# Performance work log

Hardware: AMD Instinct MI355X
Metric: run time of the kernel (lower is better)

Reference implementation:

```python
import jax, jax.numpy as jnp
import numpy as np

EPS = 1e-8      # laplace_transform epsilon
RC = 0.5        # residual_coff
L = 2           # num_layers
NU, NB, NI, D = 100000, 30000, 50000, 128
E_UB, E_UI, E_BI = 300000, 500000, 500000


def _l2norm(x):
    # F.normalize(x, p=2, dim=1)
    n = jnp.linalg.norm(x, axis=1, keepdims=True)
    return x / jnp.maximum(n, 1e-12)


def _spmm(rows, cols, vals, feats, n):
    # sparse (COO) matmul: out[r] += vals[e] * feats[cols[e]]
    return jax.ops.segment_sum(vals[:, None] * feats[cols], rows, num_segments=n)


def _sym_norm_graph(u, v, na, nb):
    # bipartite block matrix [[0, B],[B^T, 0]] with D^-1/2 A D^-1/2 normalization
    rows = jnp.concatenate([u, v + na])
    cols = jnp.concatenate([v + na, u])
    deg = jax.ops.segment_sum(jnp.ones(rows.shape[0], jnp.float32), rows,
                              num_segments=na + nb)
    dinv = 1.0 / (jnp.sqrt(deg) + EPS)
    vals = dinv[rows] * dinv[cols]
    return rows, cols, vals


def _one_propagate(rows, cols, vals, afeat, bfeat):
    n = afeat.shape[0] + bfeat.shape[0]
    feats = jnp.concatenate([afeat, bfeat], axis=0)
    ini = _l2norm(feats)
    acc = feats  # all_feats starts with raw feats, summed at the end
    for i in range(L):
        feats = _spmm(rows, cols, vals, feats, n)
        feats = (feats + RC * ini) / (i + 2)
        feats = _l2norm(feats)
        acc = acc + feats
    return acc[:afeat.shape[0]], acc[afeat.shape[0]:]


def setup_inputs() -> dict:
    key = jax.random.key(0)
    ks = jax.random.split(key, 10)
    return {
        "users_feat": jax.random.normal(ks[0], (NU, D), jnp.float32) * 0.1,
        "bundles_feat": jax.random.normal(ks[1], (NB, D), jnp.float32) * 0.1,
        "items_feat": jax.random.normal(ks[2], (NI, D), jnp.float32) * 0.1,
        "bi_vals": jax.random.uniform(ks[3], (E_BI,), jnp.float32),
        "ub_u": jax.random.randint(ks[4], (E_UB,), 0, NU),
        "ub_b": jax.random.randint(ks[5], (E_UB,), 0, NB),
        "ui_u": jax.random.randint(ks[6], (E_UI,), 0, NU),
        "ui_i": jax.random.randint(ks[7], (E_UI,), 0, NI),
        "bi_b": jax.random.randint(ks[8], (E_BI,), 0, NB),
        "bi_i": jax.random.randint(ks[9], (E_BI,), 0, NI),
    }


def reference(users_feat, bundles_feat, items_feat, bi_vals,
              ub_u, ub_b, ui_u, ui_i, bi_b, bi_i):
    nu, nb, ni = users_feat.shape[0], bundles_feat.shape[0], items_feat.shape[0]
    # UB (history) propagation
    r, c, v = _sym_norm_graph(ub_u, ub_b, nu, nb)
    hist_users, hist_bundles = _one_propagate(r, c, v, users_feat, bundles_feat)
    # UI (affinity) propagation
    r, c, v = _sym_norm_graph(ui_u, ui_i, nu, ni)
    aff_users, ui_items = _one_propagate(r, c, v, users_feat, items_feat)
    # BI aggregation: bundles x items sparse graph @ item features
    aff_bundles = _spmm(bi_b, bi_i, bi_vals, ui_items, nb)
    # concat [aff_users, hist_users, aff_bundles, hist_bundles] along rows
    return jnp.concatenate([aff_users, hist_users, aff_bundles, hist_bundles], axis=0)
```

## Files before the change

kernel.cpp:

```cpp
#include <hip/hip_runtime.h>

#define FD   128
#define FDH  64
#define EPSN 1e-8f
#define RCC  0.5f
#define SCAN_TPB 256
#define SCAN_ELEMS 1024

typedef unsigned int uint;
typedef unsigned short u16;
typedef unsigned char u8;
typedef float fx2 __attribute__((ext_vector_type(2)));

__device__ __forceinline__ float wave_sum(float x) {
#pragma unroll
    for (int off = 32; off > 0; off >>= 1) x += __shfl_xor(x, off);
    return x;
}

__device__ __forceinline__ uint packbf2(float a, float b) {
    uint ua = __float_as_uint(a); ua += 0x7fffu + ((ua >> 16) & 1u);
    uint ub = __float_as_uint(b); ub += 0x7fffu + ((ub >> 16) & 1u);
    return (ua >> 16) | (ub & 0xffff0000u);
}
__device__ __forceinline__ float2 unpackbf2(uint v) {
    return make_float2(__uint_as_float(v << 16), __uint_as_float(v & 0xffff0000u));
}
__device__ __forceinline__ u16 packfp8(float a, float b) {
    return (u16)__builtin_amdgcn_cvt_pk_fp8_f32(a, b, 0, false);
}

__global__ void passA(const int* __restrict__ ub_u, const int* __restrict__ ub_b,
                      const int* __restrict__ ui_u, const int* __restrict__ ui_i,
                      const int* __restrict__ bi_b, const int* __restrict__ bi_i,
                      const float* __restrict__ uf, const float* __restrict__ bf,
                      const float* __restrict__ itf,
                      int E_UB, int E_UI, int E_BI, int NU, int NB, int n1, int n2, int NT,
                      int nblk_edges,
                      int* __restrict__ head, int2* __restrict__ pairLL,
                      uint* __restrict__ fini16, float* __restrict__ normf) {
    if ((int)blockIdx.x < nblk_edges) {
        int e = blockIdx.x * blockDim.x + threadIdx.x;
        if (e < E_UB) {
            int a = ub_u[e], b = ub_b[e] + NU;
            int s0 = 2 * e;
            int p0 = atomicExch(&head[a], s0);
            int p1 = atomicExch(&head[b], s0 + 1);
            ((int4*)pairLL)[e] = make_int4(p0, b, p1, a);
        } else if (e < E_UB + E_UI) {
            int f = e - E_UB;
            int a = ui_u[f], bl = ui_i[f] + NU;
            int s0 = 2 * E_UB + 2 * f;
            int p0 = atomicExch(&head[n1 + a], s0);
            int p1 = atomicExch(&head[n1 + bl], s0 + 1);
            ((int4*)pairLL)[E_UB + f] = make_int4(p0, bl, p1, a);
        } else if (e < E_UB + E_UI + E_BI) {
            int g = e - E_UB - E_UI;
            int s = 2 * E_UB + 2 * E_UI + g;
            int p = atomicExch(&head[n1 + n2 + bi_b[g]], s);
            pairLL[s] = make_int2(p, bi_i[g]);
        }
    } else {
        int w = (((int)blockIdx.x - nblk_edges) * blockDim.x + threadIdx.x) >> 6;
        int lane = threadIdx.x & 63;
        if (w >= NT) return;
        const float* src = (w < NU) ? uf + (size_t)w * FD
                         : (w < NU + NB) ? bf + (size_t)(w - NU) * FD
                         : itf + (size_t)(w - NU - NB) * FD;
        float2 x = ((const float2*)src)[lane];
        float ss = wave_sum(x.x * x.x + x.y * x.y);
        float nrm = sqrtf(ss);
        float inv = 1.0f / fmaxf(nrm, 1e-12f);
        fini16[(size_t)w * FDH + lane] = packbf2(x.x * inv, x.y * inv);
        if (lane == 0) normf[w] = nrm;
    }
}

__global__ void passB(const int* __restrict__ head, const int2* __restrict__ pairLL,
                      int NN, int n12, int* __restrict__ deg, float* __restrict__ dinv) {
    int r = blockIdx.x * blockDim.x + threadIdx.x;
    if (r > NN) return;
    if (r == NN) { deg[NN] = 0; return; }
    int c = 0;
    int s = head[r];
    while (s >= 0) { c++; s = pairLL[s].x; }
    deg[r] = c;
    if (r < n12) dinv[r] = 1.0f / (sqrtf((float)c) + EPSN);
}

__global__ void conv_g8(const uint* __restrict__ fini16, const float* __restrict__ normf,
                        const float* __restrict__ dinv,
                        int n1, int NU, int NB, int n12, u16* __restrict__ g8) {
    int w = (blockIdx.x * blockDim.x + threadIdx.x) >> 6;
    int lane = threadIdx.x & 63;
    if (w >= n12) return;
    int node = (w < n1) ? w : ((w - n1 < NU) ? (w - n1) : (w - n1 + NB));
    float sc = dinv[w] * normf[node];
    float2 f = unpackbf2(fini16[(size_t)node * FDH + lane]);
    g8[(size_t)w * FDH + lane] = packfp8(f.x * sc, f.y * sc);
}

__global__ void scan_a(const int* __restrict__ in, int* __restrict__ out,
                       int* __restrict__ bsum, int nelem) {
    __shared__ int tsum[SCAN_TPB];
    int tid = threadIdx.x;
    int base = blockIdx.x * SCAN_ELEMS + tid * 4;
    int v0 = (base + 0 < nelem) ? in[base + 0] : 0;
    int v1 = (base + 1 < nelem) ? in[base + 1] : 0;
    int v2 = (base + 2 < nelem) ? in[base + 2] : 0;
    int v3 = (base + 3 < nelem) ? in[base + 3] : 0;
    int s = v0 + v1 + v2 + v3;
    tsum[tid] = s;
    __syncthreads();
    for (int off = 1; off < SCAN_TPB; off <<= 1) {
        int y = (tid >= off) ? tsum[tid - off] : 0;
        __syncthreads();
        tsum[tid] += y;
        __syncthreads();
    }
    int excl = tsum[tid] - s;
    if (tid == SCAN_TPB - 1) bsum[blockIdx.x] = tsum[SCAN_TPB - 1];
    if (base + 0 < nelem) out[base + 0] = excl;
    excl += v0;
    if (base + 1 < nelem) out[base + 1] = excl;
    excl += v1;
    if (base + 2 < nelem) out[base + 2] = excl;
    excl += v2;
    if (base + 3 < nelem) out[base + 3] = excl;
}

__global__ void scan_b(int* __restrict__ bsum, int nb) {
    __shared__ int sm[512];
    int tid = threadIdx.x;
    int v = (tid < nb) ? bsum[tid] : 0;
    sm[tid] = v;
    __syncthreads();
    for (int off = 1; off < 512; off <<= 1) {
        int y = (tid >= off) ? sm[tid - off] : 0;
        __syncthreads();
        sm[tid] += y;
        __syncthreads();
    }
    if (tid < nb) bsum[tid] = sm[tid] - v;
}

__global__ void scan_c(int* __restrict__ out, const int* __restrict__ bsum, int nelem) {
    int base = blockIdx.x * SCAN_ELEMS + threadIdx.x * 4;
    int add = bsum[blockIdx.x];
#pragma unroll
    for (int k = 0; k < 4; ++k)
        if (base + k < nelem) out[base + k] += add;
}

__global__ void passC(const int* __restrict__ head, const int2* __restrict__ pairLL,
                      const int* __restrict__ rowptr, const float* __restrict__ bi_vals,
                      int NN, int n12, int S1,
                      int* __restrict__ cols, float* __restrict__ wts) {
    int r = blockIdx.x * blockDim.x + threadIdx.x;
    if (r >= NN) return;
    int pos = rowptr[r];
    int s = head[r];
    if (r < n12) {
        while (s >= 0) { int2 p = pairLL[s]; cols[pos++] = p.y << 7; s = p.x; }
    } else {
        while (s >= 0) {
            int2 p = pairLL[s];
            cols[pos] = p.y << 8;
            wts[pos - S1] = bi_vals[s - S1];
            pos++; s = p.x;
        }
    }
}

#define GATHER_FP8(TAB)                                                          \
    float a0 = 0.f, a1 = 0.f, a2 = 0.f, a3 = 0.f;                                \
    for (int cs = s; cs < e; cs += 64) {                                         \
        int cnt = e - cs; if (cnt > 64) cnt = 64;                                \
        int colv = (lane < cnt) ? cols[cs + lane] : 0;                           \
        int p = 0;                                                               \
        for (; 2 * p + 8 <= cnt; p += 4) {                                       \
            int o0 = __shfl(colv, 2 * p + h);                                    \
            int o1 = __shfl(colv, 2 * p + 2 + h);                                \
            int o2 = __shfl(colv, 2 * p + 4 + h);                                \
            int o3 = __shfl(colv, 2 * p + 6 + h);                                \
            uint x0 = *(const uint*)(TAB + o0);                                  \
            uint x1 = *(const uint*)(TAB + o1);                                  \
            uint x2 = *(const uint*)(TAB + o2);                                  \
            uint x3 = *(const uint*)(TAB + o3);                                  \
            fx2 p0 = __builtin_amdgcn_cvt_pk_f32_fp8((int)x0, false);            \
            fx2 r0 = __builtin_amdgcn_cvt_pk_f32_fp8((int)x0, true);             \
            fx2 p1 = __builtin_amdgcn_cvt_pk_f32_fp8((int)x1, false);            \
            fx2 r1 = __builtin_amdgcn_cvt_pk_f32_fp8((int)x1, true);             \
            fx2 p2 = __builtin_amdgcn_cvt_pk_f32_fp8((int)x2, false);            \
            fx2 r2 = __builtin_amdgcn_cvt_pk_f32_fp8((int)x2, true);             \
            fx2 p3 = __builtin_amdgcn_cvt_pk_f32_fp8((int)x3, false);            \
            fx2 r3 = __builtin_amdgcn_cvt_pk_f32_fp8((int)x3, true);             \
            a0 += p0.x + p1.x + p2.x + p3.x;                                     \
            a1 += p0.y + p1.y + p2.y + p3.y;                                     \
            a2 += r0.x + r1.x + r2.x + r3.x;                                     \
            a3 += r0.y + r1.y + r2.y + r3.y;                                     \
        }                                                                        \
        for (; 2 * p + 2 <= cnt; ++p) {                                          \
            int o = __shfl(colv, 2 * p + h);                                     \
            uint x = *(const uint*)(TAB + o);                                    \
            fx2 pp = __builtin_amdgcn_cvt_pk_f32_fp8((int)x, false);             \
            fx2 rr = __builtin_amdgcn_cvt_pk_f32_fp8((int)x, true);              \
            a0 += pp.x; a1 += pp.y; a2 += rr.x; a3 += rr.y;                      \
        }                                                                        \
        if (2 * p < cnt) {                                                       \
            int o = __shfl(colv, 2 * p);                                         \
            if (h == 0) {                                                        \
                uint x = *(const uint*)(TAB + o);                                \
                fx2 pp = __builtin_amdgcn_cvt_pk_f32_fp8((int)x, false);         \
                fx2 rr = __builtin_amdgcn_cvt_pk_f32_fp8((int)x, true);          \
                a0 += pp.x; a1 += pp.y; a2 += rr.x; a3 += rr.y;                  \
            }                                                                    \
        }                                                                        \
    }                                                                            \
    a0 += __shfl_xor(a0, 32); a1 += __shfl_xor(a1, 32);                          \
    a2 += __shfl_xor(a2, 32); a3 += __shfl_xor(a3, 32);

__global__ void spmm_L1(const int* __restrict__ rowptr, const int* __restrict__ cols,
                        const float* __restrict__ dinv, const float* __restrict__ normf,
                        const uint* __restrict__ fini16, const u16* __restrict__ g8,
                        uint* __restrict__ facc16, uint* __restrict__ fX8,
                        int n1, int NU, int NB, int n12) {
    int w = (blockIdx.x * blockDim.x + threadIdx.x) >> 6;
    int lane = threadIdx.x & 63;
    if (w >= n12) return;
    int h = lane >> 5, q = lane & 31;
    int s = rowptr[w], e = rowptr[w + 1];
    bool ui = (w >= n1);
    int node = ui ? ((w - n1 < NU) ? (w - n1) : (w - n1 + NB)) : w;
    float dr = dinv[w];
    uint2 iu = ((const uint2*)(fini16 + (size_t)node * FDH))[q];
    float nr = normf[node];
    const u8* tab = (const u8*)g8 + ((size_t)(ui ? n1 : 0) << 7) + (q << 2);
    GATHER_FP8(tab)
    float2 i01 = unpackbf2(iu.x), i23 = unpackbf2(iu.y);
    float v0 = (dr * a0 + RCC * i01.x) * 0.5f;
    float v1 = (dr * a1 + RCC * i01.y) * 0.5f;
    float v2 = (dr * a2 + RCC * i23.x) * 0.5f;
    float v3 = (dr * a3 + RCC * i23.y) * 0.5f;
    float sq = v0 * v0 + v1 * v1 + v2 * v2 + v3 * v3;
#pragma unroll
    for (int off = 16; off > 0; off >>= 1) sq += __shfl_xor(sq, off);
    float inv = 1.0f / fmaxf(sqrtf(sq), 1e-12f);
    v0 *= inv; v1 *= inv; v2 *= inv; v3 *= inv;
    if (h == 0) {
        uint2 fa;
        fa.x = packbf2(fmaf(i01.x, nr, v0), fmaf(i01.y, nr, v1));
        fa.y = packbf2(fmaf(i23.x, nr, v2), fmaf(i23.y, nr, v3));
        ((uint2*)(facc16 + (size_t)w * FDH))[q] = fa;
        int xu = __builtin_amdgcn_cvt_pk_fp8_f32(v0 * dr, v1 * dr, 0, false);
        xu = __builtin_amdgcn_cvt_pk_fp8_f32(v2 * dr, v3 * dr, xu, true);
        fX8[(size_t)w * 32 + q] = (uint)xu;
    }
}

__global__ void spmm_L2(const int* __restrict__ rowptr, const int* __restrict__ cols,
                        const float* __restrict__ dinv, const uint* __restrict__ fini16,
                        const uint* __restrict__ facc16, const uint* __restrict__ fX8,
                        uint* __restrict__ items16, float* __restrict__ outp,
                        int n1, int NU, int NB, int n12) {
    int w = (blockIdx.x * blockDim.x + threadIdx.x) >> 6;
    int lane = threadIdx.x & 63;
    if (w >= n12) return;
    int h = lane >> 5, q = lane & 31;
    int s = rowptr[w], e = rowptr[w + 1];
    bool ui = (w >= n1);
    int node = ui ? ((w - n1 < NU) ? (w - n1) : (w - n1 + NB)) : w;
    float dr = dinv[w];
    uint2 iu = ((const uint2*)(fini16 + (size_t)node * FDH))[q];
    uint2 au = ((const uint2*)(facc16 + (size_t)w * FDH))[q];
    const u8* tab = (const u8*)fX8 + ((size_t)(ui ? n1 : 0) << 7) + (q << 2);
    GATHER_FP8(tab)
    float2 i01 = unpackbf2(iu.x), i23 = unpackbf2(iu.y);
    float v0 = (dr * a0 + RCC * i01.x) * (1.0f / 3.0f);
    float v1 = (dr * a1 + RCC * i01.y) * (1.0f / 3.0f);
    float v2 = (dr * a2 + RCC * i23.x) * (1.0f / 3.0f);
    float v3 = (dr * a3 + RCC * i23.y) * (1.0f / 3.0f);
    float sq = v0 * v0 + v1 * v1 + v2 * v2 + v3 * v3;
#pragma unroll
    for (int off = 16; off > 0; off >>= 1) sq += __shfl_xor(sq, off);
    float inv = 1.0f / fmaxf(sqrtf(sq), 1e-12f);
    v0 *= inv; v1 *= inv; v2 *= inv; v3 *= inv;
    float2 a01 = unpackbf2(au.x), a23 = unpackbf2(au.y);
    float n0 = a01.x + v0, o1v = a01.y + v1, n2v = a23.x + v2, n3 = a23.y + v3;
    if (h == 0) {
        if (!ui) {
            size_t dst = (w < NU) ? (size_t)(NU + w) : (size_t)(2 * NU + NB + (w - NU));
            ((float4*)(outp + dst * FD))[q] = make_float4(n0, o1v, n2v, n3);
        } else {
            int l = w - n1;
            if (l < NU) {
                ((float4*)(outp + (size_t)l * FD))[q] = make_float4(n0, o1v, n2v, n3);
            } else {
                uint2 it;
                it.x = packbf2(n0, o1v);
                it.y = packbf2(n2v, n3);
                ((uint2*)(items16 + (size_t)(l - NU) * FDH))[q] = it;
            }
        }
    }
}

__global__ void bi_gather(const int* __restrict__ rowptr, const int* __restrict__ cols,
                          const float* __restrict__ wts, int S1,
                          const uint* __restrict__ items16,
                          float* __restrict__ outb, int nb) {
    int w = (blockIdx.x * blockDim.x + threadIdx.x) >> 6;
    int lane = threadIdx.x & 63;
    if (w >= nb) return;
    int h = lane >> 5, q = lane & 31;
    int s = rowptr[w], e = rowptr[w + 1];
    const u8* tab = (const u8*)items16 + (q << 3);
    float a0 = 0.f, a1 = 0.f, a2 = 0.f, a3 = 0.f;
    for (int cs = s; cs < e; cs += 64) {
        int cnt = e - cs; if (cnt > 64) cnt = 64;
        int colv = (lane < cnt) ? cols[cs + lane] : 0;
        float wtv = (lane < cnt) ? wts[cs + lane - S1] : 0.0f;
        int p = 0;
        for (; 2 * p + 8 <= cnt; p += 4) {
            int o0 = __shfl(colv, 2 * p + h);
            int o1 = __shfl(colv, 2 * p + 2 + h);
            int o2 = __shfl(colv, 2 * p + 4 + h);
            int o3 = __shfl(colv, 2 * p + 6 + h);
            float w0 = __shfl(wtv, 2 * p + h);
            float w1 = __shfl(wtv, 2 * p + 2 + h);
            float w2 = __shfl(wtv, 2 * p + 4 + h);
            float w3 = __shfl(wtv, 2 * p + 6 + h);
            uint2 x0 = *(const uint2*)(tab + o0);
            uint2 x1 = *(const uint2*)(tab + o1);
            uint2 x2 = *(const uint2*)(tab + o2);
            uint2 x3 = *(const uint2*)(tab + o3);
            float2 f;
            f = unpackbf2(x0.x); a0 = fmaf(w0, f.x, a0); a1 = fmaf(w0, f.y, a1);
            f = unpackbf2(x0.y); a2 = fmaf(w0, f.x, a2); a3 = fmaf(w0, f.y, a3);
            f = unpackbf2(x1.x); a0 = fmaf(w1, f.x, a0); a1 = fmaf(w1, f.y, a1);
            f = unpackbf2(x1.y); a2 = fmaf(w1, f.x, a2); a3 = fmaf(w1, f.y, a3);
            f = unpackbf2(x2.x); a0 = fmaf(w2, f.x, a0); a1 = fmaf(w2, f.y, a1);
            f = unpackbf2(x2.y); a2 = fmaf(w2, f.x, a2); a3 = fmaf(w2, f.y, a3);
            f = unpackbf2(x3.x); a0 = fmaf(w3, f.x, a0); a1 = fmaf(w3, f.y, a1);
            f = unpackbf2(x3.y); a2 = fmaf(w3, f.x, a2); a3 = fmaf(w3, f.y, a3);
        }
        for (; 2 * p + 2 <= cnt; ++p) {
            int o = __shfl(colv, 2 * p + h);
            float wt = __shfl(wtv, 2 * p + h);
            uint2 x = *(const uint2*)(tab + o);
            float2 f;
            f = unpackbf2(x.x); a0 = fmaf(wt, f.x, a0); a1 = fmaf(wt, f.y, a1);
            f = unpackbf2(x.y); a2 = fmaf(wt, f.x, a2); a3 = fmaf(wt, f.y, a3);
        }
        if (2 * p < cnt) {
            int o = __shfl(colv, 2 * p);
            float wt = __shfl(wtv, 2 * p);
            if (h == 0) {
                uint2 x = *(const uint2*)(tab + o);
                float2 f;
                f = unpackbf2(x.x); a0 = fmaf(wt, f.x, a0); a1 = fmaf(wt, f.y, a1);
                f = unpackbf2(x.y); a2 = fmaf(wt, f.x, a2); a3 = fmaf(wt, f.y, a3);
            }
        }
    }
    a0 += __shfl_xor(a0, 32); a1 += __shfl_xor(a1, 32);
    a2 += __shfl_xor(a2, 32); a3 += __shfl_xor(a3, 32);
    if (h == 0)
        ((float4*)(outb + (size_t)w * FD))[q] = make_float4(a0, a1, a2, a3);
}

extern "C" void kernel_launch(void* const* d_in, const int* in_sizes, int n_in,
                              void* d_out, int out_size, void* d_ws, size_t ws_size,
                              hipStream_t stream) {
    const float* users   = (const float*)d_in[0];
    const float* bundles = (const float*)d_in[1];
    const float* items   = (const float*)d_in[2];
    const float* bi_vals = (const float*)d_in[3];
    const int* ub_u = (const int*)d_in[4];
    const int* ub_b = (const int*)d_in[5];
    const int* ui_u = (const int*)d_in[6];
    const int* ui_i = (const int*)d_in[7];
    const int* bi_b = (const int*)d_in[8];
    const int* bi_i = (const int*)d_in[9];

    const int NU = in_sizes[0] / FD;
    const int NB = in_sizes[1] / FD;
    const int NI = in_sizes[2] / FD;
    const int E_BI = in_sizes[3];
    const int E_UB = in_sizes[4];
    const int E_UI = in_sizes[6];
    float* out = (float*)d_out;

    const int n1 = NU + NB, n2 = NU + NI;
    const int n12 = n1 + n2;
    const int NT = NU + NB + NI;
    const int NN = n12 + NB;
    const int S1 = 2 * E_UB + 2 * E_UI;
    const int TOT = S1 + E_BI;
    const int ETOT = E_UB + E_UI + E_BI;

    uint* fini16   = (uint*)d_ws;
    uint* facc16   = fini16 + (size_t)NT * FDH;
    uint* items16  = facc16 + (size_t)n12 * FDH;
    u16* g8        = (u16*)(items16 + (size_t)NI * FDH);
    uint* fX8      = (uint*)(g8 + (size_t)n12 * FDH);
    float* normf   = (float*)(fX8 + (size_t)n12 * 32);
    float* dinv    = normf + NT;
    float* wts     = dinv + n12;
    int* deg       = (int*)(wts + E_BI);
    int* rowptr    = deg + (NN + 1);
    int* head      = rowptr + (NN + 1);
    int* bsum      = head + NN;
    int* cols      = bsum + 512;
    int2* pairLL   = (int2*)((((size_t)(cols + TOT)) + 15) & ~(size_t)15);

    dim3 blk(256);
    auto rows_grid = [](int n) { return dim3((unsigned)((n + 3) / 4)); };
    auto thr_grid  = [](int n) { return dim3((unsigned)((n + 255) / 256)); };

    hipMemsetAsync(head, 0xFF, (size_t)NN * 4, stream);
    int nblk_edges = (ETOT + 255) / 256;
    int nblk_prep  = (NT + 3) / 4;
    passA<<<dim3((unsigned)(nblk_edges + nblk_prep)), blk, 0, stream>>>(
        ub_u, ub_b, ui_u, ui_i, bi_b, bi_i, users, bundles, items,
        E_UB, E_UI, E_BI, NU, NB, n1, n2, NT, nblk_edges,
        head, pairLL, fini16, normf);
    passB<<<thr_grid(NN + 1), blk, 0, stream>>>(head, pairLL, NN, n12, deg, dinv);
    conv_g8<<<rows_grid(n12), blk, 0, stream>>>(fini16, normf, dinv, n1, NU, NB, n12, g8);
    {
        int nelem = NN + 1;
        int nblk = (nelem + SCAN_ELEMS - 1) / SCAN_ELEMS;
        scan_a<<<dim3((unsigned)nblk), dim3(SCAN_TPB), 0, stream>>>(deg, rowptr, bsum, nelem);
        scan_b<<<dim3(1), dim3(512), 0, stream>>>(bsum, nblk);
        scan_c<<<dim3((unsigned)nblk), dim3(SCAN_TPB), 0, stream>>>(rowptr, bsum, nelem);
    }
    passC<<<thr_grid(NN), blk, 0, stream>>>(head, pairLL, rowptr, bi_vals,
                                            NN, n12, S1, cols, wts);

    spmm_L1<<<rows_grid(n12), blk, 0, stream>>>(rowptr, cols, dinv, normf,
                                                fini16, g8, facc16, fX8, n1, NU, NB, n12);
    spmm_L2<<<rows_grid(n12), blk, 0, stream>>>(rowptr, cols, dinv, fini16,
                                                facc16, fX8, items16, out, n1, NU, NB, n12);
    bi_gather<<<rows_grid(NB), blk, 0, stream>>>(rowptr + n12, cols, wts, S1, items16,
        out + (size_t)2 * NU * FD, NB);
}
```

Before: 675.9 us.

## Process two rows per wavefront, fuse conv_g8 into passC, pack BI cols+weights

```diff
diff --git a/kernel.cpp b/kernel.cpp
--- a/kernel.cpp
+++ b/kernel.cpp
@@ -88,18 +88,6 @@
     if (r < n12) dinv[r] = 1.0f / (sqrtf((float)c) + EPSN);
 }
 
-__global__ void conv_g8(const uint* __restrict__ fini16, const float* __restrict__ normf,
-                        const float* __restrict__ dinv,
-                        int n1, int NU, int NB, int n12, u16* __restrict__ g8) {
-    int w = (blockIdx.x * blockDim.x + threadIdx.x) >> 6;
-    int lane = threadIdx.x & 63;
-    if (w >= n12) return;
-    int node = (w < n1) ? w : ((w - n1 < NU) ? (w - n1) : (w - n1 + NB));
-    float sc = dinv[w] * normf[node];
-    float2 f = unpackbf2(fini16[(size_t)node * FDH + lane]);
-    g8[(size_t)w * FDH + lane] = packfp8(f.x * sc, f.y * sc);
-}
-
 __global__ void scan_a(const int* __restrict__ in, int* __restrict__ out,
                        int* __restrict__ bsum, int nelem) {
     __shared__ int tsum[SCAN_TPB];
@@ -152,109 +140,127 @@
         if (base + k < nelem) out[base + k] += add;
 }
 
-__global__ void passC(const int* __restrict__ head, const int2* __restrict__ pairLL,
-                      const int* __restrict__ rowptr, const float* __restrict__ bi_vals,
-                      int NN, int n12, int S1,
-                      int* __restrict__ cols, float* __restrict__ wts) {
-    int r = blockIdx.x * blockDim.x + threadIdx.x;
-    if (r >= NN) return;
-    int pos = rowptr[r];
-    int s = head[r];
-    if (r < n12) {
-        while (s >= 0) { int2 p = pairLL[s]; cols[pos++] = p.y << 7; s = p.x; }
+__global__ void passC_conv(const int* __restrict__ head, const int2* __restrict__ pairLL,
+                           const int* __restrict__ rowptr, const float* __restrict__ bi_vals,
+                           int NN, int n12, int S1,
+                           int* __restrict__ cols, int2* __restrict__ bi2,
+                           const uint* __restrict__ fini16, const float* __restrict__ normf,
+                           const float* __restrict__ dinv,
+                           int n1, int NU, int NB, u16* __restrict__ g8, int nblkC) {
+    if ((int)blockIdx.x < nblkC) {
+        int r = blockIdx.x * blockDim.x + threadIdx.x;
+        if (r >= NN) return;
+        int pos = rowptr[r];
+        int s = head[r];
+        if (r < n12) {
+            while (s >= 0) { int2 p = pairLL[s]; cols[pos++] = p.y << 7; s = p.x; }
+        } else {
+            while (s >= 0) {
+                int2 p = pairLL[s];
+                bi2[pos - S1] = make_int2(p.y << 8, __float_as_int(bi_vals[s - S1]));
+                pos++; s = p.x;
+            }
+        }
     } else {
-        while (s >= 0) {
-            int2 p = pairLL[s];
-            cols[pos] = p.y << 8;
-            wts[pos - S1] = bi_vals[s - S1];
-            pos++; s = p.x;
-        }
-    }
-}
-
-#define GATHER_FP8(TAB)                                                          \
-    float a0 = 0.f, a1 = 0.f, a2 = 0.f, a3 = 0.f;                                \
-    for (int cs = s; cs < e; cs += 64) {                                         \
-        int cnt = e - cs; if (cnt > 64) cnt = 64;                                \
-        int colv = (lane < cnt) ? cols[cs + lane] : 0;                           \
+        int w = (((int)blockIdx.x - nblkC) * blockDim.x + threadIdx.x) >> 6;
+        int lane = threadIdx.x & 63;
+        if (w >= n12) return;
+        int node = (w < n1) ? w : ((w - n1 < NU) ? (w - n1) : (w - n1 + NB));
+        float sc = dinv[w] * normf[node];
+        float2 f = unpackbf2(fini16[(size_t)node * FDH + lane]);
+        g8[(size_t)w * FDH + lane] = packfp8(f.x * sc, f.y * sc);
+    }
+}
+
+#define ACC8(XU)  {                                                              \
+    fx2 _pa = __builtin_amdgcn_cvt_pk_f32_fp8((int)(XU).x, false);               \
+    fx2 _pb = __builtin_amdgcn_cvt_pk_f32_fp8((int)(XU).x, true);                \
+    fx2 _pc = __builtin_amdgcn_cvt_pk_f32_fp8((int)(XU).y, false);               \
+    fx2 _pd = __builtin_amdgcn_cvt_pk_f32_fp8((int)(XU).y, true);                \
+    a0 += _pa.x; a1 += _pa.y; a2 += _pb.x; a3 += _pb.y;                          \
+    a4 += _pc.x; a5 += _pc.y; a6 += _pd.x; a7 += _pd.y; }
+
+#define GATHER8(TAB)                                                             \
+    float a0=0.f,a1=0.f,a2=0.f,a3=0.f,a4=0.f,a5=0.f,a6=0.f,a7=0.f;               \
+    {                                                                            \
+      int base = lane & 32;                                                      \
+      for (int cs = s; cs < e; cs += 32) {                                       \
+        int cnt = e - cs; if (cnt > 32) cnt = 32;                                \
+        int colv = (l31 < cnt) ? cols[cs + l31] : 0;                             \
         int p = 0;                                                               \
         for (; 2 * p + 8 <= cnt; p += 4) {                                       \
-            int o0 = __shfl(colv, 2 * p + h);                                    \
-            int o1 = __shfl(colv, 2 * p + 2 + h);                                \
-            int o2 = __shfl(colv, 2 * p + 4 + h);                                \
-            int o3 = __shfl(colv, 2 * p + 6 + h);                                \
-            uint x0 = *(const uint*)(TAB + o0);                                  \
-            uint x1 = *(const uint*)(TAB + o1);                                  \
-            uint x2 = *(const uint*)(TAB + o2);                                  \
-            uint x3 = *(const uint*)(TAB + o3);                                  \
-            fx2 p0 = __builtin_amdgcn_cvt_pk_f32_fp8((int)x0, false);            \
-            fx2 r0 = __builtin_amdgcn_cvt_pk_f32_fp8((int)x0, true);             \
-            fx2 p1 = __builtin_amdgcn_cvt_pk_f32_fp8((int)x1, false);            \
-            fx2 r1 = __builtin_amdgcn_cvt_pk_f32_fp8((int)x1, true);             \
-            fx2 p2 = __builtin_amdgcn_cvt_pk_f32_fp8((int)x2, false);            \
-            fx2 r2 = __builtin_amdgcn_cvt_pk_f32_fp8((int)x2, true);             \
-            fx2 p3 = __builtin_amdgcn_cvt_pk_f32_fp8((int)x3, false);            \
-            fx2 r3 = __builtin_amdgcn_cvt_pk_f32_fp8((int)x3, true);             \
-            a0 += p0.x + p1.x + p2.x + p3.x;                                     \
-            a1 += p0.y + p1.y + p2.y + p3.y;                                     \
-            a2 += r0.x + r1.x + r2.x + r3.x;                                     \
-            a3 += r0.y + r1.y + r2.y + r3.y;                                     \
+            int o0 = __shfl(colv, base + 2 * p + sub);                           \
+            int o1 = __shfl(colv, base + 2 * p + 2 + sub);                       \
+            int o2 = __shfl(colv, base + 2 * p + 4 + sub);                       \
+            int o3 = __shfl(colv, base + 2 * p + 6 + sub);                       \
+            uint2 x0 = *(const uint2*)(TAB + o0);                                \
+            uint2 x1 = *(const uint2*)(TAB + o1);                                \
+            uint2 x2 = *(const uint2*)(TAB + o2);                                \
+            uint2 x3 = *(const uint2*)(TAB + o3);                                \
+            ACC8(x0) ACC8(x1) ACC8(x2) ACC8(x3)                                  \
         }                                                                        \
         for (; 2 * p + 2 <= cnt; ++p) {                                          \
-            int o = __shfl(colv, 2 * p + h);                                     \
-            uint x = *(const uint*)(TAB + o);                                    \
-            fx2 pp = __builtin_amdgcn_cvt_pk_f32_fp8((int)x, false);             \
-            fx2 rr = __builtin_amdgcn_cvt_pk_f32_fp8((int)x, true);              \
-            a0 += pp.x; a1 += pp.y; a2 += rr.x; a3 += rr.y;                      \
+            int o = __shfl(colv, base + 2 * p + sub);                            \
+            uint2 x = *(const uint2*)(TAB + o);                                  \
+            ACC8(x)                                                              \
         }                                                                        \
         if (2 * p < cnt) {                                                       \
-            int o = __shfl(colv, 2 * p);                                         \
-            if (h == 0) {                                                        \
-                uint x = *(const uint*)(TAB + o);                                \
-                fx2 pp = __builtin_amdgcn_cvt_pk_f32_fp8((int)x, false);         \
-                fx2 rr = __builtin_amdgcn_cvt_pk_f32_fp8((int)x, true);          \
-                a0 += pp.x; a1 += pp.y; a2 += rr.x; a3 += rr.y;                  \
-            }                                                                    \
+            int o = __shfl(colv, base + 2 * p);                                  \
+            if (sub == 0) { uint2 x = *(const uint2*)(TAB + o); ACC8(x) }        \
         }                                                                        \
+      }                                                                          \
     }                                                                            \
-    a0 += __shfl_xor(a0, 32); a1 += __shfl_xor(a1, 32);                          \
-    a2 += __shfl_xor(a2, 32); a3 += __shfl_xor(a3, 32);
+    a0 += __shfl_xor(a0, 16); a1 += __shfl_xor(a1, 16);                          \
+    a2 += __shfl_xor(a2, 16); a3 += __shfl_xor(a3, 16);                          \
+    a4 += __shfl_xor(a4, 16); a5 += __shfl_xor(a5, 16);                          \
+    a6 += __shfl_xor(a6, 16); a7 += __shfl_xor(a7, 16);
 
 __global__ void spmm_L1(const int* __restrict__ rowptr, const int* __restrict__ cols,
                         const float* __restrict__ dinv, const float* __restrict__ normf,
                         const uint* __restrict__ fini16, const u16* __restrict__ g8,
                         uint* __restrict__ facc16, uint* __restrict__ fX8,
                         int n1, int NU, int NB, int n12) {
-    int w = (blockIdx.x * blockDim.x + threadIdx.x) >> 6;
+    int wv = (blockIdx.x * blockDim.x + threadIdx.x) >> 6;
     int lane = threadIdx.x & 63;
-    if (w >= n12) return;
-    int h = lane >> 5, q = lane & 31;
-    int s = rowptr[w], e = rowptr[w + 1];
-    bool ui = (w >= n1);
-    int node = ui ? ((w - n1 < NU) ? (w - n1) : (w - n1 + NB)) : w;
-    float dr = dinv[w];
-    uint2 iu = ((const uint2*)(fini16 + (size_t)node * FDH))[q];
+    int hw = lane >> 5, l31 = lane & 31, sub = (lane >> 4) & 1, t = lane & 15;
+    int r = 2 * wv + hw;
+    if (r >= n12) return;
+    int s = rowptr[r], e = rowptr[r + 1];
+    bool ui = (r >= n1);
+    int node = ui ? ((r - n1 < NU) ? (r - n1) : (r - n1 + NB)) : r;
+    float dr = dinv[r];
+    uint4 iu = ((const uint4*)(fini16 + (size_t)node * FDH))[t];
     float nr = normf[node];
-    const u8* tab = (const u8*)g8 + ((size_t)(ui ? n1 : 0) << 7) + (q << 2);
-    GATHER_FP8(tab)
+    const u8* tab = (const u8*)g8 + ((size_t)(ui ? n1 : 0) << 7) + (t << 3);
+    GATHER8(tab)
     float2 i01 = unpackbf2(iu.x), i23 = unpackbf2(iu.y);
+    float2 i45 = unpackbf2(iu.z), i67 = unpackbf2(iu.w);
     float v0 = (dr * a0 + RCC * i01.x) * 0.5f;
     float v1 = (dr * a1 + RCC * i01.y) * 0.5f;
     float v2 = (dr * a2 + RCC * i23.x) * 0.5f;
     float v3 = (dr * a3 + RCC * i23.y) * 0.5f;
-    float sq = v0 * v0 + v1 * v1 + v2 * v2 + v3 * v3;
+    float v4 = (dr * a4 + RCC * i45.x) * 0.5f;
+    float v5 = (dr * a5 + RCC * i45.y) * 0.5f;
+    float v6 = (dr * a6 + RCC * i67.x) * 0.5f;
+    float v7 = (dr * a7 + RCC * i67.y) * 0.5f;
+    float sq = v0*v0 + v1*v1 + v2*v2 + v3*v3 + v4*v4 + v5*v5 + v6*v6 + v7*v7;
 #pragma unroll
-    for (int off = 16; off > 0; off >>= 1) sq += __shfl_xor(sq, off);
+    for (int off = 8; off > 0; off >>= 1) sq += __shfl_xor(sq, off);
     float inv = 1.0f / fmaxf(sqrtf(sq), 1e-12f);
     v0 *= inv; v1 *= inv; v2 *= inv; v3 *= inv;
-    if (h == 0) {
-        uint2 fa;
+    v4 *= inv; v5 *= inv; v6 *= inv; v7 *= inv;
+    if (sub == 0) {
+        uint4 fa;
         fa.x = packbf2(fmaf(i01.x, nr, v0), fmaf(i01.y, nr, v1));
         fa.y = packbf2(fmaf(i23.x, nr, v2), fmaf(i23.y, nr, v3));
-        ((uint2*)(facc16 + (size_t)w * FDH))[q] = fa;
-        int xu = __builtin_amdgcn_cvt_pk_fp8_f32(v0 * dr, v1 * dr, 0, false);
-        xu = __builtin_amdgcn_cvt_pk_fp8_f32(v2 * dr, v3 * dr, xu, true);
-        fX8[(size_t)w * 32 + q] = (uint)xu;
+        fa.z = packbf2(fmaf(i45.x, nr, v4), fmaf(i45.y, nr, v5));
+        fa.w = packbf2(fmaf(i67.x, nr, v6), fmaf(i67.y, nr, v7));
+        ((uint4*)(facc16 + (size_t)r * FDH))[t] = fa;
+        int xa = __builtin_amdgcn_cvt_pk_fp8_f32(v0 * dr, v1 * dr, 0, false);
+        xa = __builtin_amdgcn_cvt_pk_fp8_f32(v2 * dr, v3 * dr, xa, true);
+        int xb = __builtin_amdgcn_cvt_pk_fp8_f32(v4 * dr, v5 * dr, 0, false);
+        xb = __builtin_amdgcn_cvt_pk_fp8_f32(v6 * dr, v7 * dr, xb, true);
+        ((uint2*)(fX8 + (size_t)r * 32))[t] = make_uint2((uint)xa, (uint)xb);
     }
 }
 
@@ -263,110 +269,121 @@
                         const uint* __restrict__ facc16, const uint* __restrict__ fX8,
                         uint* __restrict__ items16, float* __restrict__ outp,
                         int n1, int NU, int NB, int n12) {
-    int w = (blockIdx.x * blockDim.x + threadIdx.x) >> 6;
+    int wv = (blockIdx.x * blockDim.x + threadIdx.x) >> 6;
     int lane = threadIdx.x & 63;
-    if (w >= n12) return;
-    int h = lane >> 5, q = lane & 31;
-    int s = rowptr[w], e = rowptr[w + 1];
-    bool ui = (w >= n1);
-    int node = ui ? ((w - n1 < NU) ? (w - n1) : (w - n1 + NB)) : w;
-    float dr = dinv[w];
-    uint2 iu = ((const uint2*)(fini16 + (size_t)node * FDH))[q];
-    uint2 au = ((const uint2*)(facc16 + (size_t)w * FDH))[q];
-    const u8* tab = (const u8*)fX8 + ((size_t)(ui ? n1 : 0) << 7) + (q << 2);
-    GATHER_FP8(tab)
+    int hw = lane >> 5, l31 = lane & 31, sub = (lane >> 4) & 1, t = lane & 15;
+    int r = 2 * wv + hw;
+    if (r >= n12) return;
+    int s = rowptr[r], e = rowptr[r + 1];
+    bool ui = (r >= n1);
+    int node = ui ? ((r - n1 < NU) ? (r - n1) : (r - n1 + NB)) : r;
+    float dr = dinv[r];
+    uint4 iu = ((const uint4*)(fini16 + (size_t)node * FDH))[t];
+    uint4 au = ((const uint4*)(facc16 + (size_t)r * FDH))[t];
+    const u8* tab = (const u8*)fX8 + ((size_t)(ui ? n1 : 0) << 7) + (t << 3);
+    GATHER8(tab)
     float2 i01 = unpackbf2(iu.x), i23 = unpackbf2(iu.y);
+    float2 i45 = unpackbf2(iu.z), i67 = unpackbf2(iu.w);
     float v0 = (dr * a0 + RCC * i01.x) * (1.0f / 3.0f);
     float v1 = (dr * a1 + RCC * i01.y) * (1.0f / 3.0f);
     float v2 = (dr * a2 + RCC * i23.x) * (1.0f / 3.0f);
     float v3 = (dr * a3 + RCC * i23.y) * (1.0f / 3.0f);
-    float sq = v0 * v0 + v1 * v1 + v2 * v2 + v3 * v3;
+    float v4 = (dr * a4 + RCC * i45.x) * (1.0f / 3.0f);
+    float v5 = (dr * a5 + RCC * i45.y) * (1.0f / 3.0f);
+    float v6 = (dr * a6 + RCC * i67.x) * (1.0f / 3.0f);
+    float v7 = (dr * a7 + RCC * i67.y) * (1.0f / 3.0f);
+    float sq = v0*v0 + v1*v1 + v2*v2 + v3*v3 + v4*v4 + v5*v5 + v6*v6 + v7*v7;
 #pragma unroll
-    for (int off = 16; off > 0; off >>= 1) sq += __shfl_xor(sq, off);
+    for (int off = 8; off > 0; off >>= 1) sq += __shfl_xor(sq, off);
     float inv = 1.0f / fmaxf(sqrtf(sq), 1e-12f);
     v0 *= inv; v1 *= inv; v2 *= inv; v3 *= inv;
+    v4 *= inv; v5 *= inv; v6 *= inv; v7 *= inv;
     float2 a01 = unpackbf2(au.x), a23 = unpackbf2(au.y);
-    float n0 = a01.x + v0, o1v = a01.y + v1, n2v = a23.x + v2, n3 = a23.y + v3;
-    if (h == 0) {
+    float2 a45 = unpackbf2(au.z), a67 = unpackbf2(au.w);
+    float n0 = a01.x + v0, n1v = a01.y + v1, n2v = a23.x + v2, n3 = a23.y + v3;
+    float n4 = a45.x + v4, n5 = a45.y + v5, n6 = a67.x + v6, n7 = a67.y + v7;
+    if (sub == 0) {
         if (!ui) {
-            size_t dst = (w < NU) ? (size_t)(NU + w) : (size_t)(2 * NU + NB + (w - NU));
-            ((float4*)(outp + dst * FD))[q] = make_float4(n0, o1v, n2v, n3);
+            size_t dst = (r < NU) ? (size_t)(NU + r) : (size_t)(2 * NU + NB + (r - NU));
+            float* orow = outp + dst * FD;
+            ((float4*)orow)[2 * t]     = make_float4(n0, n1v, n2v, n3);
+            ((float4*)orow)[2 * t + 1] = make_float4(n4, n5, n6, n7);
         } else {
-            int l = w - n1;
+            int l = r - n1;
             if (l < NU) {
-                ((float4*)(outp + (size_t)l * FD))[q] = make_float4(n0, o1v, n2v, n3);
+                float* orow = outp + (size_t)l * FD;
+                ((float4*)orow)[2 * t]     = make_float4(n0, n1v, n2v, n3);
+                ((float4*)orow)[2 * t + 1] = make_float4(n4, n5, n6, n7);
             } else {
-                uint2 it;
-                it.x = packbf2(n0, o1v);
+                uint4 it;
+                it.x = packbf2(n0, n1v);
                 it.y = packbf2(n2v, n3);
-                ((uint2*)(items16 + (size_t)(l - NU) * FDH))[q] = it;
+                it.z = packbf2(n4, n5);
+                it.w = packbf2(n6, n7);
+                ((uint4*)(items16 + (size_t)(l - NU) * FDH))[t] = it;
             }
         }
     }
 }
 
-__global__ void bi_gather(const int* __restrict__ rowptr, const int* __restrict__ cols,
-                          const float* __restrict__ wts, int S1,
-                          const uint* __restrict__ items16,
+#define FMA8(XU, W) { float2 _f;                                                 \
+    _f = unpackbf2((XU).x); a0 = fmaf(W, _f.x, a0); a1 = fmaf(W, _f.y, a1);      \
+    _f = unpackbf2((XU).y); a2 = fmaf(W, _f.x, a2); a3 = fmaf(W, _f.y, a3);      \
+    _f = unpackbf2((XU).z); a4 = fmaf(W, _f.x, a4); a5 = fmaf(W, _f.y, a5);      \
+    _f = unpackbf2((XU).w); a6 = fmaf(W, _f.x, a6); a7 = fmaf(W, _f.y, a7); }
+
+__global__ void bi_gather(const int* __restrict__ rowptr, const int2* __restrict__ bi2,
+                          int S1, const uint* __restrict__ items16,
                           float* __restrict__ outb, int nb) {
-    int w = (blockIdx.x * blockDim.x + threadIdx.x) >> 6;
+    int wv = (blockIdx.x * blockDim.x + threadIdx.x) >> 6;
     int lane = threadIdx.x & 63;
-    if (w >= nb) return;
-    int h = lane >> 5, q = lane & 31;
-    int s = rowptr[w], e = rowptr[w + 1];
-    const u8* tab = (const u8*)items16 + (q << 3);
-    float a0 = 0.f, a1 = 0.f, a2 = 0.f, a3 = 0.f;
-    for (int cs = s; cs < e; cs += 64) {
-        int cnt = e - cs; if (cnt > 64) cnt = 64;
-        int colv = (lane < cnt) ? cols[cs + lane] : 0;
-        float wtv = (lane < cnt) ? wts[cs + lane - S1] : 0.0f;
+    int hw = lane >> 5, l31 = lane & 31, sub = (lane >> 4) & 1, t = lane & 15;
+    int r = 2 * wv + hw;
+    if (r >= nb) return;
+    int s = rowptr[r], e = rowptr[r + 1];
+    const u8* tab = (const u8*)items16 + (t << 4);
+    float a0=0.f,a1=0.f,a2=0.f,a3=0.f,a4=0.f,a5=0.f,a6=0.f,a7=0.f;
+    int base = lane & 32;
+    for (int cs = s; cs < e; cs += 32) {
+        int cnt = e - cs; if (cnt > 32) cnt = 32;
+        int2 cv = (l31 < cnt) ? bi2[cs + l31 - S1] : make_int2(0, 0);
         int p = 0;
         for (; 2 * p + 8 <= cnt; p += 4) {
-            int o0 = __shfl(colv, 2 * p + h);
-            int o1 = __shfl(colv, 2 * p + 2 + h);
-            int o2 = __shfl(colv, 2 * p + 4 + h);
-            int o3 = __shfl(colv, 2 * p + 6 + h);
-            float w0 = __shfl(wtv, 2 * p + h);
-            float w1 = __shfl(wtv, 2 * p + 2 + h);
-            float w2 = __shfl(wtv, 2 * p + 4 + h);
-            float w3 = __shfl(wtv, 2 * p + 6 + h);
-            uint2 x0 = *(const uint2*)(tab + o0);
-            uint2 x1 = *(const uint2*)(tab + o1);
-            uint2 x2 = *(const uint2*)(tab + o2);
-            uint2 x3 = *(const uint2*)(tab + o3);
-            float2 f;
-            f = unpackbf2(x0.x); a0 = fmaf(w0, f.x, a0); a1 = fmaf(w0, f.y, a1);
-            f = unpackbf2(x0.y); a2 = fmaf(w0, f.x, a2); a3 = fmaf(w0, f.y, a3);
-            f = unpackbf2(x1.x); a0 = fmaf(w1, f.x, a0); a1 = fmaf(w1, f.y, a1);
-            f = unpackbf2(x1.y); a2 = fmaf(w1, f.x, a2); a3 = fmaf(w1, f.y, a3);
-            f = unpackbf2(x2.x); a0 = fmaf(w2, f.x, a0); a1 = fmaf(w2, f.y, a1);
-            f = unpackbf2(x2.y); a2 = fmaf(w2, f.x, a2); a3 = fmaf(w2, f.y, a3);
-            f = unpackbf2(x3.x); a0 = fmaf(w3, f.x, a0); a1 = fmaf(w3, f.y, a1);
-            f = unpackbf2(x3.y); a2 = fmaf(w3, f.x, a2); a3 = fmaf(w3, f.y, a3);
+            int o0 = __shfl(cv.x, base + 2 * p + sub);
+            int o1 = __shfl(cv.x, base + 2 * p + 2 + sub);
+            int o2 = __shfl(cv.x, base + 2 * p + 4 + sub);
+            int o3 = __shfl(cv.x, base + 2 * p + 6 + sub);
+            float w0 = __int_as_float(__shfl(cv.y, base + 2 * p + sub));
+            float w1 = __int_as_float(__shfl(cv.y, base + 2 * p + 2 + sub));
+            float w2 = __int_as_float(__shfl(cv.y, base + 2 * p + 4 + sub));
+            float w3 = __int_as_float(__shfl(cv.y, base + 2 * p + 6 + sub));
+            uint4 x0 = *(const uint4*)(tab + o0);
+            uint4 x1 = *(const uint4*)(tab + o1);
+            uint4 x2 = *(const uint4*)(tab + o2);
+            uint4 x3 = *(const uint4*)(tab + o3);
+            FMA8(x0, w0) FMA8(x1, w1) FMA8(x2, w2) FMA8(x3, w3)
         }
         for (; 2 * p + 2 <= cnt; ++p) {
-            int o = __shfl(colv, 2 * p + h);
-            float wt = __shfl(wtv, 2 * p + h);
-            uint2 x = *(const uint2*)(tab + o);
-            float2 f;
-            f = unpackbf2(x.x); a0 = fmaf(wt, f.x, a0); a1 = fmaf(wt, f.y, a1);
-            f = unpackbf2(x.y); a2 = fmaf(wt, f.x, a2); a3 = fmaf(wt, f.y, a3);
+            int o = __shfl(cv.x, base + 2 * p + sub);
+            float wt = __int_as_float(__shfl(cv.y, base + 2 * p + sub));
+            uint4 x = *(const uint4*)(tab + o);
+            FMA8(x, wt)
         }
         if (2 * p < cnt) {
-            int o = __shfl(colv, 2 * p);
-            float wt = __shfl(wtv, 2 * p);
-            if (h == 0) {
-                uint2 x = *(const uint2*)(tab + o);
-                float2 f;
-                f = unpackbf2(x.x); a0 = fmaf(wt, f.x, a0); a1 = fmaf(wt, f.y, a1);
-                f = unpackbf2(x.y); a2 = fmaf(wt, f.x, a2); a3 = fmaf(wt, f.y, a3);
-            }
-        }
-    }
-    a0 += __shfl_xor(a0, 32); a1 += __shfl_xor(a1, 32);
-    a2 += __shfl_xor(a2, 32); a3 += __shfl_xor(a3, 32);
-    if (h == 0)
-        ((float4*)(outb + (size_t)w * FD))[q] = make_float4(a0, a1, a2, a3);
+            int o = __shfl(cv.x, base + 2 * p);
+            float wt = __int_as_float(__shfl(cv.y, base + 2 * p));
+            if (sub == 0) { uint4 x = *(const uint4*)(tab + o); FMA8(x, wt) }
+        }
+    }
+    a0 += __shfl_xor(a0, 16); a1 += __shfl_xor(a1, 16);
+    a2 += __shfl_xor(a2, 16); a3 += __shfl_xor(a3, 16);
+    a4 += __shfl_xor(a4, 16); a5 += __shfl_xor(a5, 16);
+    a6 += __shfl_xor(a6, 16); a7 += __shfl_xor(a7, 16);
+    if (sub == 0) {
+        float* orow = outb + (size_t)r * FD;
+        ((float4*)orow)[2 * t]     = make_float4(a0, a1, a2, a3);
+        ((float4*)orow)[2 * t + 1] = make_float4(a4, a5, a6, a7);
+    }
 }
 
 extern "C" void kernel_launch(void* const* d_in, const int* in_sizes, int n_in,
@@ -406,17 +423,18 @@
     uint* fX8      = (uint*)(g8 + (size_t)n12 * FDH);
     float* normf   = (float*)(fX8 + (size_t)n12 * 32);
     float* dinv    = normf + NT;
-    float* wts     = dinv + n12;
-    int* deg       = (int*)(wts + E_BI);
+    int* deg       = (int*)(dinv + n12);
     int* rowptr    = deg + (NN + 1);
     int* head      = rowptr + (NN + 1);
     int* bsum      = head + NN;
     int* cols      = bsum + 512;
-    int2* pairLL   = (int2*)((((size_t)(cols + TOT)) + 15) & ~(size_t)15);
+    int2* bi2      = (int2*)((((size_t)(cols + S1)) + 15) & ~(size_t)15);
+    int2* pairLL   = (int2*)((((size_t)(bi2 + E_BI)) + 15) & ~(size_t)15);
 
     dim3 blk(256);
-    auto rows_grid = [](int n) { return dim3((unsigned)((n + 3) / 4)); };
-    auto thr_grid  = [](int n) { return dim3((unsigned)((n + 255) / 256)); };
+    auto rows_grid  = [](int n) { return dim3((unsigned)((n + 3) / 4)); };
+    auto rows2_grid = [](int n) { return dim3((unsigned)((n + 7) / 8)); };
+    auto thr_grid   = [](int n) { return dim3((unsigned)((n + 255) / 256)); };
 
     hipMemsetAsync(head, 0xFF, (size_t)NN * 4, stream);
     int nblk_edges = (ETOT + 255) / 256;
@@ -426,7 +444,6 @@
         E_UB, E_UI, E_BI, NU, NB, n1, n2, NT, nblk_edges,
         head, pairLL, fini16, normf);
     passB<<<thr_grid(NN + 1), blk, 0, stream>>>(head, pairLL, NN, n12, deg, dinv);
-    conv_g8<<<rows_grid(n12), blk, 0, stream>>>(fini16, normf, dinv, n1, NU, NB, n12, g8);
     {
         int nelem = NN + 1;
         int nblk = (nelem + SCAN_ELEMS - 1) / SCAN_ELEMS;
@@ -434,13 +451,18 @@
         scan_b<<<dim3(1), dim3(512), 0, stream>>>(bsum, nblk);
         scan_c<<<dim3((unsigned)nblk), dim3(SCAN_TPB), 0, stream>>>(rowptr, bsum, nelem);
     }
-    passC<<<thr_grid(NN), blk, 0, stream>>>(head, pairLL, rowptr, bi_vals,
-                                            NN, n12, S1, cols, wts);
-
-    spmm_L1<<<rows_grid(n12), blk, 0, stream>>>(rowptr, cols, dinv, normf,
-                                                fini16, g8, facc16, fX8, n1, NU, NB, n12);
-    spmm_L2<<<rows_grid(n12), blk, 0, stream>>>(rowptr, cols, dinv, fini16,
-                                                facc16, fX8, items16, out, n1, NU, NB, n12);
-    bi_gather<<<rows_grid(NB), blk, 0, stream>>>(rowptr + n12, cols, wts, S1, items16,
+    {
+        int nblkC = (NN + 255) / 256;
+        int nblkG = (n12 + 3) / 4;
+        passC_conv<<<dim3((unsigned)(nblkC + nblkG)), blk, 0, stream>>>(
+            head, pairLL, rowptr, bi_vals, NN, n12, S1, cols, bi2,
+            fini16, normf, dinv, n1, NU, NB, g8, nblkC);
+    }
+
+    spmm_L1<<<rows2_grid(n12), blk, 0, stream>>>(rowptr, cols, dinv, normf,
+                                                 fini16, g8, facc16, fX8, n1, NU, NB, n12);
+    spmm_L2<<<rows2_grid(n12), blk, 0, stream>>>(rowptr, cols, dinv, fini16,
+                                                 facc16, fX8, items16, out, n1, NU, NB, n12);
+    bi_gather<<<rows2_grid(NB), blk, 0, stream>>>(rowptr + n12, bi2, S1, items16,
         out + (size_t)2 * NU * FD, NB);
 }
```

Result: faster. 601.8 us (-11.0%).
